# Kernel tuning notes

Hardware: AMD Instinct MI355X
Metric: run time of the kernel (lower is better)

## Reference

```python
import jax, jax.numpy as jnp
import numpy as np
from jax import lax

P = 8  # DFFN patch_size


def _ln(x, w, b):
    # WithBias LayerNorm over channel dim of NCHW (matches to_3d -> LN(-1) -> to_4d)
    mu = x.mean(1, keepdims=True)
    var = ((x - mu) ** 2).mean(1, keepdims=True)
    return (x - mu) / jnp.sqrt(var + 1e-5) * w[None, :, None, None] + b[None, :, None, None]


def _conv1x1(x, w, b=None):
    y = jnp.einsum('bchw,oc->bohw', x, w)
    if b is not None:
        y = y + b[None, :, None, None]
    return y


def setup_inputs() -> dict:
    key = jax.random.key(0)
    ks = jax.random.split(key, 9)
    B, C, H, W = 2, 64, 96, 96
    hid = C  # ffn_expansion_factor = 1
    s = lambda k, shape, scale=0.05: jax.random.normal(k, shape, jnp.float32) * scale
    return {
        'x': s(ks[0], (B, C, H, W), 1.0),
        'ln1_w': jnp.ones((C,), jnp.float32), 'ln1_b': jnp.zeros((C,), jnp.float32),
        'ln2_w': jnp.ones((C,), jnp.float32), 'ln2_b': jnp.zeros((C,), jnp.float32),
        'q_w': s(ks[1], (C, C)), 'q_b': jnp.zeros((C,), jnp.float32),
        'k_w': s(ks[2], (C, C)), 'k_b': jnp.zeros((C,), jnp.float32),
        'v_w': s(ks[3], (C, C)), 'v_b': jnp.zeros((C,), jnp.float32),
        'fft_w': s(ks[4], (hid, P, P // 2 + 1), 1.0),
        'proj_in_w': s(ks[5], (hid, C)),
        'dw_w': s(ks[6], (hid, 1, 3, 3)),
        'proj_out_w': s(ks[7], (C, hid // 2)),
    }


def reference(x, ln1_w, ln1_b, ln2_w, ln2_b, q_w, q_b, k_w, k_b, v_w, v_b,
              fft_w, proj_in_w, dw_w, proj_out_w):
    B, C, H, W = x.shape
    # --- attention sub-block (unscaled spatial self-attn) ---
    xn = _ln(x, ln1_w, ln1_b)
    q = _conv1x1(xn, q_w, q_b).reshape(B, C, H * W)
    k = _conv1x1(xn, k_w, k_b).reshape(B, C, H * W)
    v = _conv1x1(xn, v_w, v_b).reshape(B, C, H * W)
    attn = jax.nn.softmax(jnp.einsum('bcn,bcm->bnm', q, k), axis=-1)  # [B, HW, HW]
    out = jnp.einsum('bcm,bnm->bcn', v, attn).reshape(B, C, H, W)
    x = x + out
    # --- DFFN sub-block ---
    xn = _ln(x, ln2_w, ln2_b)
    h = _conv1x1(xn, proj_in_w)  # hidden == C (expansion factor 1)
    hid = h.shape[1]
    hb, wb = H // P, W // P
    hp = h.reshape(B, hid, hb, P, wb, P).transpose(0, 2, 4, 1, 3, 5)  # [B,hb,wb,hid,P,P]
    hf = jnp.fft.rfft2(hp) * fft_w  # real learned spectral filter
    hp = jnp.fft.irfft2(hf, s=(P, P))
    h = hp.transpose(0, 3, 1, 4, 2, 5).reshape(B, hid, H, W)
    h = lax.conv_general_dilated(h, dw_w, (1, 1), ((1, 1), (1, 1)),
                                 feature_group_count=hid,
                                 dimension_numbers=('NCHW', 'OIHW', 'NCHW'))
    h1, h2 = jnp.split(h, 2, axis=1)
    h = jax.nn.gelu(h1, approximate=False) * h2  # torch F.gelu is exact erf
    return x + _conv1x1(h, proj_out_w)
```

## Files before the change

kernel.cpp:

```cpp
#include <hip/hip_runtime.h>
#include <hip/hip_bf16.h>
#include <math.h>

#define CH 64
#define NPOS 9216
#define NTOT 18432
#define NSPLIT 12
#define TILES_PER_SPLIT 12
#define LOG2E 1.4426950408889634f

typedef short bf16x8 __attribute__((ext_vector_type(8)));
typedef short bf16x4 __attribute__((ext_vector_type(4)));
typedef float f32x4 __attribute__((ext_vector_type(4)));
typedef int   i32x4 __attribute__((ext_vector_type(4)));
typedef int   i32x2 __attribute__((ext_vector_type(2)));
typedef unsigned int u32;

__device__ __forceinline__ float bf2f(short s) {
  unsigned int u = ((unsigned int)(unsigned short)s) << 16;
  return __builtin_bit_cast(float, u);
}
__device__ __forceinline__ short f2bf(float f) {
  unsigned int u = __builtin_bit_cast(unsigned int, f);
  unsigned int r = (u + 0x7fffu + ((u >> 16) & 1u)) >> 16;
  return (short)r;
}
__device__ __forceinline__ float gelu_exact(float x) {
  return 0.5f * x * (1.f + erff(x * 0.70710678118654752440f));
}


__global__ __launch_bounds__(256) void k_ln_qkv(
    const float* __restrict__ x, const float* __restrict__ ln1w, const float* __restrict__ ln1b,
    const float* __restrict__ qw, const float* __restrict__ qb,
    const float* __restrict__ kw, const float* __restrict__ kb,
    const float* __restrict__ vw, const float* __restrict__ vb,
    short* __restrict__ Qg, short* __restrict__ Kg, short* __restrict__ Vgt) {
  __shared__ float s1a[256], s2a[256];
  __shared__ __align__(16) short xn[32 * 72];
  int t = threadIdx.x;
  int w8 = t >> 5;
  int p = t & 31;
  int q0 = blockIdx.x * 32;
  int q = q0 + p;
  int b = q / NPOS;
  int nn = q0 % NPOS;
  int n = q % NPOS;

  const float* xb = x + (size_t)b * CH * NPOS + n;
  float xr[8];
  float s1 = 0.f, s2 = 0.f;
#pragma unroll
  for (int cl = 0; cl < 8; ++cl) {
    float v = xb[(size_t)(w8 * 8 + cl) * NPOS];
    xr[cl] = v;
    s1 += v;
    s2 += v * v;
  }
  s1a[w8 * 32 + p] = s1;
  s2a[w8 * 32 + p] = s2;
  __syncthreads();
  float mu = 0.f, m2 = 0.f;
#pragma unroll
  for (int ww = 0; ww < 8; ++ww) { mu += s1a[ww * 32 + p]; m2 += s2a[ww * 32 + p]; }
  mu *= (1.f / 64.f);
  float var = m2 * (1.f / 64.f) - mu * mu;
  float rstd = rsqrtf(var + 1e-5f);
  {
    u32* xw = (u32*)xn;
#pragma unroll
    for (int j2 = 0; j2 < 4; ++j2) {
      int cl = 2 * j2, c = w8 * 8 + cl;
      float y0 = (xr[cl] - mu) * rstd * ln1w[c] + ln1b[c];
      float y1 = (xr[cl + 1] - mu) * rstd * ln1w[c + 1] + ln1b[c + 1];
      u32 pk = ((u32)(unsigned short)f2bf(y1) << 16) | (u32)(unsigned short)f2bf(y0);
      xw[p * 36 + w8 * 4 + j2] = pk;
    }
  }
  __syncthreads();
  int lane = t & 63;
  int L = lane & 15, quad = lane >> 4;
  int cs = t >> 6;
  bf16x8 b0[2], b1[2];
#pragma unroll
  for (int ps = 0; ps < 2; ++ps) {
    b0[ps] = *(const bf16x8*)(xn + (ps * 16 + L) * 72 + quad * 8);
    b1[ps] = *(const bf16x8*)(xn + (ps * 16 + L) * 72 + 32 + quad * 8);
  }
#pragma unroll
  for (int m = 0; m < 3; ++m) {
    const float* wsrc = (m == 0) ? qw : (m == 1) ? kw : vw;
    const float* bsrc = (m == 0) ? qb : (m == 1) ? kb : vb;
    bf16x8 a0, a1;
    {
      const float* wr = wsrc + (cs * 16 + L) * 64 + quad * 8;
#pragma unroll
      for (int j = 0; j < 8; ++j) { a0[j] = f2bf(wr[j]); a1[j] = f2bf(wr[32 + j]); }
    }
    float bi[4];
#pragma unroll
    for (int i = 0; i < 4; ++i) bi[i] = bsrc[cs * 16 + quad * 4 + i];
#pragma unroll
    for (int ps = 0; ps < 2; ++ps) {
      f32x4 acc = {bi[0], bi[1], bi[2], bi[3]};
      acc = __builtin_amdgcn_mfma_f32_16x16x32_bf16(a0, b0[ps], acc, 0, 0, 0);
      acc = __builtin_amdgcn_mfma_f32_16x16x32_bf16(a1, b1[ps], acc, 0, 0, 0);
      int idx = b * NPOS + nn + ps * 16 + L;
      if (m == 0) {
#pragma unroll
        for (int i = 0; i < 4; ++i)
          Qg[(size_t)idx * 64 + cs * 16 + quad * 4 + i] = f2bf(acc[i]);
      } else if (m == 1) {
#pragma unroll
        for (int i = 0; i < 4; ++i)
          Kg[(size_t)idx * 64 + cs * 16 + quad * 4 + i] = f2bf(acc[i] * LOG2E);
      } else {
#pragma unroll
        for (int i = 0; i < 4; ++i)
          Vgt[(size_t)(cs * 16 + quad * 4 + i) * NTOT + idx] = f2bf(acc[i]);
      }
    }
  }
}

#define LDPK 80
#define LDP  72
__global__ __launch_bounds__(512) void k_attn(
    const short* __restrict__ Qg, const short* __restrict__ Kg, const short* __restrict__ Vgt,
    u32* __restrict__ PoT, float* __restrict__ Pl) {
  __shared__ __align__(16) short Kt[2][64 * LDPK];
  __shared__ __align__(16) short Vt[2][64 * LDP];
  int b = blockIdx.y;
  int n0 = blockIdx.x * 256;
  int ks = blockIdx.z;
  int tid = threadIdx.x;
  int w = tid >> 6, lane = tid & 63;
  int L = lane & 15, quad = lane >> 4;

  bf16x8 qa[2][2];
#pragma unroll
  for (int qt = 0; qt < 2; ++qt) {
    const short* qb_ = Qg + ((size_t)(b * NPOS + n0 + w * 32 + qt * 16 + L)) * 64;
    qa[qt][0] = *(const bf16x8*)(qb_ + quad * 8);
    qa[qt][1] = *(const bf16x8*)(qb_ + 32 + quad * 8);
  }

  f32x4 o[2][4];
#pragma unroll
  for (int qt = 0; qt < 2; ++qt)
#pragma unroll
    for (int nb = 0; nb < 4; ++nb) o[qt][nb] = (f32x4){0.f, 0.f, 0.f, 0.f};
  float rl[2] = {0.f, 0.f};

  int ck = tid & 7, rk = tid >> 3;
  int c8 = tid & 7, dr = tid >> 3;
  int vslot = (c8 >> 2) * 32 + (c8 & 1) * 16 + ((c8 >> 1) & 1) * 4;
  i32x4 kr, vr;
  {
    int kt = ks * TILES_PER_SPLIT;
    kr = ((const i32x4*)(Kg + ((size_t)(b * NPOS + kt * 64)) * 64))[tid];
    vr = *(const i32x4*)(Vgt + (size_t)b * NPOS + kt * 64 + c8 * 8 + (size_t)dr * NTOT);
    ((i32x4*)Kt[0])[rk * 10 + ck] = kr;
    short* vrow = Vt[0] + dr * LDP + vslot;
    *(i32x2*)(vrow) = (i32x2){vr[0], vr[1]};
    *(i32x2*)(vrow + 8) = (i32x2){vr[2], vr[3]};
  }

  for (int t = 0; t < TILES_PER_SPLIT; ++t) {
    int cur = t & 1;
    if (t + 1 < TILES_PER_SPLIT) {
      int kt = ks * TILES_PER_SPLIT + t + 1;
      kr = ((const i32x4*)(Kg + ((size_t)(b * NPOS + kt * 64)) * 64))[tid];
      vr = *(const i32x4*)(Vgt + (size_t)b * NPOS + kt * 64 + c8 * 8 + (size_t)dr * NTOT);
    }
    __syncthreads();

    const i32x4* kt4 = (const i32x4*)Kt[cur];
    const short* vt = Vt[cur];
    __builtin_amdgcn_s_setprio(1);
#pragma unroll
    for (int kp = 0; kp < 2; ++kp) {
      u32 pw0[4], pw1[4];
#pragma unroll
      for (int h = 0; h < 2; ++h) {
        int kti = kp * 2 + h;
        bf16x8 kf0 = __builtin_bit_cast(bf16x8, kt4[(kti * 16 + L) * 10 + quad]);
        bf16x8 kf1 = __builtin_bit_cast(bf16x8, kt4[(kti * 16 + L) * 10 + 4 + quad]);
#pragma unroll
        for (int qt = 0; qt < 2; ++qt) {
          f32x4 st = {0.f, 0.f, 0.f, 0.f};
          st = __builtin_amdgcn_mfma_f32_16x16x32_bf16(kf0, qa[qt][0], st, 0, 0, 0);
          st = __builtin_amdgcn_mfma_f32_16x16x32_bf16(kf1, qa[qt][1], st, 0, 0, 0);
          float p0 = __builtin_amdgcn_exp2f(st[0]);
          float p1 = __builtin_amdgcn_exp2f(st[1]);
          float p2 = __builtin_amdgcn_exp2f(st[2]);
          float p3 = __builtin_amdgcn_exp2f(st[3]);
          rl[qt] += (p0 + p1) + (p2 + p3);
          u32 lo = __builtin_amdgcn_perm(__builtin_bit_cast(u32, p1), __builtin_bit_cast(u32, p0), 0x07060302u);
          u32 hi = __builtin_amdgcn_perm(__builtin_bit_cast(u32, p3), __builtin_bit_cast(u32, p2), 0x07060302u);
          if (qt == 0) { pw0[h * 2] = lo; pw0[h * 2 + 1] = hi; }
          else         { pw1[h * 2] = lo; pw1[h * 2 + 1] = hi; }
        }
      }
      i32x4 pq0 = {(int)pw0[0], (int)pw0[1], (int)pw0[2], (int)pw0[3]};
      i32x4 pq1 = {(int)pw1[0], (int)pw1[1], (int)pw1[2], (int)pw1[3]};
      bf16x8 pp0 = __builtin_bit_cast(bf16x8, pq0);
      bf16x8 pp1 = __builtin_bit_cast(bf16x8, pq1);
#pragma unroll
      for (int nb = 0; nb < 4; ++nb) {
        bf16x8 va8 = *(const bf16x8*)(vt + (nb * 16 + L) * LDP + kp * 32 + quad * 8);
        o[0][nb] = __builtin_amdgcn_mfma_f32_16x16x32_bf16(va8, pp0, o[0][nb], 0, 0, 0);
        o[1][nb] = __builtin_amdgcn_mfma_f32_16x16x32_bf16(va8, pp1, o[1][nb], 0, 0, 0);
      }
    }
    __builtin_amdgcn_s_setprio(0);

    if (t + 1 < TILES_PER_SPLIT) {
      int nxt = 1 - cur;
      ((i32x4*)Kt[nxt])[rk * 10 + ck] = kr;
      short* vrow = Vt[nxt] + dr * LDP + vslot;
      *(i32x2*)(vrow) = (i32x2){vr[0], vr[1]};
      *(i32x2*)(vrow + 8) = (i32x2){vr[2], vr[3]};
    }
  }

#pragma unroll
  for (int qt = 0; qt < 2; ++qt) {
    rl[qt] += __shfl_xor(rl[qt], 16);
    rl[qt] += __shfl_xor(rl[qt], 32);
  }

#pragma unroll
  for (int qt = 0; qt < 2; ++qt) {
    int qg = b * NPOS + n0 + w * 32 + qt * 16 + L;
#pragma unroll
    for (int nb = 0; nb < 4; ++nb)
#pragma unroll
      for (int ip = 0; ip < 2; ++ip) {
        u32 pk = ((u32)(unsigned short)f2bf(o[qt][nb][2 * ip + 1]) << 16) |
                 (u32)(unsigned short)f2bf(o[qt][nb][2 * ip]);
        int d32 = nb * 8 + quad * 2 + ip;
        PoT[((size_t)(ks * 32 + d32)) * NTOT + qg] = pk;
      }
    if (quad == 0) Pl[(size_t)ks * NTOT + qg] = rl[qt];
  }
}

__global__ __launch_bounds__(256) void k_res_ln2_proj(
    const float* __restrict__ x, const u32* __restrict__ PoT, const float* __restrict__ Pl,
    const float* __restrict__ ln2w, const float* __restrict__ ln2b,
    const float* __restrict__ piw,
    float* __restrict__ X2, float* __restrict__ Hbuf) {
  __shared__ float s1a[32 * 32], s2a[32 * 32];
  __shared__ float inva[32], mua[32], rsa[32];
  __shared__ __align__(16) short xn[32 * 72];
  int t = threadIdx.x;
  int q0 = blockIdx.x * 32;
  int b = q0 / NPOS;
  int nn = q0 % NPOS;

  if (t < 32) {
    float ls = 0.f;
#pragma unroll
    for (int s = 0; s < NSPLIT; ++s) ls += Pl[(size_t)s * NTOT + q0 + t];
    inva[t] = 1.f / ls;
  }
  __syncthreads();

  int rho = t >> 3;
  int p4 = (t & 7) * 4;
  int c0 = rho * 2;

  float aL[4] = {0.f, 0.f, 0.f, 0.f}, aH[4] = {0.f, 0.f, 0.f, 0.f};
#pragma unroll
  for (int s = 0; s < NSPLIT; ++s) {
    i32x4 v = *(const i32x4*)(PoT + (size_t)(s * 32 + rho) * NTOT + q0 + p4);
#pragma unroll
    for (int i = 0; i < 4; ++i) {
      u32 u = (u32)v[i];
      aL[i] += __builtin_bit_cast(float, u << 16);
      aH[i] += __builtin_bit_cast(float, u & 0xffff0000u);
    }
  }
  f32x4 x0 = *(const f32x4*)(x + (size_t)b * CH * NPOS + (size_t)c0 * NPOS + nn + p4);
  f32x4 x1 = *(const f32x4*)(x + (size_t)b * CH * NPOS + (size_t)(c0 + 1) * NPOS + nn + p4);
  float v0[4], v1[4];
  f32x4 ps1, ps2;
#pragma unroll
  for (int i = 0; i < 4; ++i) {
    float iv = inva[p4 + i];
    v0[i] = x0[i] + aL[i] * iv;
    v1[i] = x1[i] + aH[i] * iv;
    ps1[i] = v0[i] + v1[i];
    ps2[i] = v0[i] * v0[i] + v1[i] * v1[i];
  }
  *(f32x4*)&s1a[rho * 32 + p4] = ps1;
  *(f32x4*)&s2a[rho * 32 + p4] = ps2;
  {
    float* xo = X2 + (size_t)b * CH * NPOS + nn + p4;
    *(f32x4*)(xo + (size_t)c0 * NPOS) = (f32x4){v0[0], v0[1], v0[2], v0[3]};
    *(f32x4*)(xo + (size_t)(c0 + 1) * NPOS) = (f32x4){v1[0], v1[1], v1[2], v1[3]};
  }
  __syncthreads();
  if (t < 32) {
    float m = 0.f, m2 = 0.f;
#pragma unroll
    for (int r = 0; r < 32; ++r) { m += s1a[r * 32 + t]; m2 += s2a[r * 32 + t]; }
    m *= (1.f / 64.f);
    float var = m2 * (1.f / 64.f) - m * m;
    mua[t] = m;
    rsa[t] = rsqrtf(var + 1e-5f);
  }
  __syncthreads();
  {
    u32* xw = (u32*)xn;
    float w0 = ln2w[c0], w1 = ln2w[c0 + 1];
    float bb0 = ln2b[c0], bb1 = ln2b[c0 + 1];
#pragma unroll
    for (int i = 0; i < 4; ++i) {
      int p = p4 + i;
      float mu = mua[p], rs = rsa[p];
      float y0 = (v0[i] - mu) * rs * w0 + bb0;
      float y1 = (v1[i] - mu) * rs * w1 + bb1;
      xw[p * 36 + rho] = ((u32)(unsigned short)f2bf(y1) << 16) | (u32)(unsigned short)f2bf(y0);
    }
  }
  __syncthreads();
  int lane = t & 63;
  int L = lane & 15, quad = lane >> 4;
  int cs = t >> 6;
  bf16x8 a0, a1;
  {
    const float* wr = piw + (cs * 16 + L) * 64 + quad * 8;
#pragma unroll
    for (int j = 0; j < 8; ++j) { a0[j] = f2bf(wr[j]); a1[j] = f2bf(wr[32 + j]); }
  }
  float* hb = Hbuf + (size_t)b * CH * NPOS + nn;
#pragma unroll
  for (int ps = 0; ps < 2; ++ps) {
    bf16x8 b0 = *(const bf16x8*)(xn + (ps * 16 + L) * 72 + quad * 8);
    bf16x8 b1 = *(const bf16x8*)(xn + (ps * 16 + L) * 72 + 32 + quad * 8);
    f32x4 acc = {0.f, 0.f, 0.f, 0.f};
    acc = __builtin_amdgcn_mfma_f32_16x16x32_bf16(a0, b0, acc, 0, 0, 0);
    acc = __builtin_amdgcn_mfma_f32_16x16x32_bf16(a1, b1, acc, 0, 0, 0);
#pragma unroll
    for (int i = 0; i < 4; ++i)
      hb[(size_t)(cs * 16 + quad * 4 + i) * NPOS + ps * 16 + L] = acc[i];
  }
}

#define LDB 100
__global__ __launch_bounds__(96) void k_conv(
    float* __restrict__ Hbuf, const float* __restrict__ fftw) {
  __shared__ __align__(16) float band[8 * LDB];
  __shared__ float kl[64];
  int hb = blockIdx.x, c = blockIdx.y, b = blockIdx.z;
  int t = threadIdx.x;
  float* base = Hbuf + (size_t)(b * CH + c) * NPOS + hb * 8 * 96;
  if (t < 64) {
    int dp = t >> 3, dq = t & 7;
    const float r = 0.70710678118654752440f;
    const float CO[8] = {1.f, r, 0.f, -r, -1.f, -r, 0.f, r};
    const float* wc = fftw + c * 40;
    float acc = 0.f;
#pragma unroll
    for (int u = 0; u < 8; ++u) {
#pragma unroll
      for (int v = 0; v < 8; ++v) {
        float wv = (v <= 4) ? wc[u * 5 + v] : wc[((8 - u) & 7) * 5 + (8 - v)];
        acc += wv * CO[(u * dp + v * dq) & 7];
      }
    }
    kl[t] = acc * (1.f / 64.f);
  }
  {
    int sr = t / 12, sc = (t % 12) * 8;
    f32x4 a = *(const f32x4*)(base + sr * 96 + sc);
    f32x4 d = *(const f32x4*)(base + sr * 96 + sc + 4);
    *(f32x4*)&band[sr * LDB + sc] = a;
    *(f32x4*)&band[sr * LDB + sc + 4] = d;
  }
  __syncthreads();
  int p = t / 12, wb = t % 12;
  float out[8] = {0.f, 0.f, 0.f, 0.f, 0.f, 0.f, 0.f, 0.f};
#pragma unroll
  for (int dp = 0; dp < 8; ++dp) {
    int rr = (p - dp) & 7;
    f32x4 a = *(const f32x4*)&band[rr * LDB + wb * 8];
    f32x4 d = *(const f32x4*)&band[rr * LDB + wb * 8 + 4];
    float v[8] = {a[0], a[1], a[2], a[3], d[0], d[1], d[2], d[3]};
    const float* krow = &kl[dp * 8];
#pragma unroll
    for (int dq = 0; dq < 8; ++dq) {
      float kv = krow[dq];
#pragma unroll
      for (int q = 0; q < 8; ++q) out[q] += kv * v[(q - dq) & 7];
    }
  }
  __syncthreads();
  f32x4 w0 = {out[0], out[1], out[2], out[3]};
  f32x4 w1 = {out[4], out[5], out[6], out[7]};
  *(f32x4*)(base + p * 96 + wb * 8) = w0;
  *(f32x4*)(base + p * 96 + wb * 8 + 4) = w1;
}

__global__ __launch_bounds__(256) void k_dw_gate(
    const float* __restrict__ Hbuf, const float* __restrict__ dww,
    float* __restrict__ G) {
  int cc = blockIdx.y;
  int q = blockIdx.x * 256 + threadIdx.x;
  int b = q / NPOS, n = q % NPOS;
  int y = n / 96, xx = n % 96;
  const float* h1 = Hbuf + (size_t)(b * CH + cc) * NPOS;
  const float* h2 = Hbuf + (size_t)(b * CH + cc + 32) * NPOS;
  float wd1[9], wd2[9];
#pragma unroll
  for (int ki = 0; ki < 9; ++ki) { wd1[ki] = dww[cc * 9 + ki]; wd2[ki] = dww[(cc + 32) * 9 + ki]; }
  float d1 = 0.f, d2 = 0.f;
  for (int dy = -1; dy <= 1; ++dy) {
    int yy = y + dy;
    if (yy < 0 || yy >= 96) continue;
    for (int dx = -1; dx <= 1; ++dx) {
      int xv = xx + dx;
      if (xv < 0 || xv >= 96) continue;
      int ki = (dy + 1) * 3 + (dx + 1);
      d1 += h1[yy * 96 + xv] * wd1[ki];
      d2 += h2[yy * 96 + xv] * wd2[ki];
    }
  }
  G[(size_t)cc * NTOT + q] = gelu_exact(d1) * d2;
}

__global__ __launch_bounds__(256) void k_proj_out(
    const float* __restrict__ G, const float* __restrict__ poww,
    const float* __restrict__ X2, float* __restrict__ out) {
  int og = blockIdx.y;
  int q = blockIdx.x * 256 + threadIdx.x;
  int b = q / NPOS, n = q % NPOS;
  float g[32];
#pragma unroll
  for (int cg = 0; cg < 32; ++cg) g[cg] = G[(size_t)cg * NTOT + q];
  const float* xr = X2 + (size_t)b * CH * NPOS + n;
  float* ob = out + (size_t)b * CH * NPOS + n;
#pragma unroll
  for (int j = 0; j < 4; ++j) {
    int oc = og * 4 + j;
    const float* prow = poww + oc * 32;
    float acc = xr[(size_t)oc * NPOS];
#pragma unroll
    for (int cg = 0; cg < 32; ++cg) acc += prow[cg] * g[cg];
    ob[(size_t)oc * NPOS] = acc;
  }
}

extern "C" void kernel_launch(void* const* d_in, const int* in_sizes, int n_in,
                              void* d_out, int out_size, void* d_ws, size_t ws_size,
                              hipStream_t stream) {
  const float* x    = (const float*)d_in[0];
  const float* ln1w = (const float*)d_in[1];
  const float* ln1b = (const float*)d_in[2];
  const float* ln2w = (const float*)d_in[3];
  const float* ln2b = (const float*)d_in[4];
  const float* qw   = (const float*)d_in[5];
  const float* qb   = (const float*)d_in[6];
  const float* kw   = (const float*)d_in[7];
  const float* kb   = (const float*)d_in[8];
  const float* vw   = (const float*)d_in[9];
  const float* vb   = (const float*)d_in[10];
  const float* fftw = (const float*)d_in[11];
  const float* piw  = (const float*)d_in[12];
  const float* dww  = (const float*)d_in[13];
  const float* poww = (const float*)d_in[14];

  short* Qg  = (short*)d_ws;
  short* Kg  = Qg + (size_t)NTOT * 64;
  short* Vgt = Kg + (size_t)NTOT * 64;
  u32*   PoT = (u32*)(Vgt + (size_t)NTOT * 64);
  float* Pl  = (float*)(PoT + (size_t)NSPLIT * 32 * NTOT);
  float* X2  = Pl + (size_t)NSPLIT * NTOT;
  float* Hbuf = X2 + (size_t)NTOT * 64;
  float* G   = Hbuf + (size_t)NTOT * 64;

  k_ln_qkv<<<dim3(576), 256, 0, stream>>>(x, ln1w, ln1b, qw, qb, kw, kb, vw, vb, Qg, Kg, Vgt);
  k_attn<<<dim3(36, 2, NSPLIT), 512, 0, stream>>>(Qg, Kg, Vgt, PoT, Pl);
  k_res_ln2_proj<<<dim3(576), 256, 0, stream>>>(x, PoT, Pl, ln2w, ln2b, piw, X2, Hbuf);
  k_conv<<<dim3(12, 64, 2), 96, 0, stream>>>(Hbuf, fftw);
  k_dw_gate<<<dim3(72, 32), 256, 0, stream>>>(Hbuf, dww, G);
  k_proj_out<<<dim3(72, 16), 256, 0, stream>>>(G, poww, X2, (float*)d_out);
}
```

Measured before the change: 169.6 us.

## Split attention tile compute around LDS prefetch store; vectorize depthwise gate

In the attention kernel, the per-tile compute is split into two halves, and the store of the prefetched next K/V tile into shared memory is placed between them. This overlaps the LDS writes with MFMA work instead of leaving them after all compute. Separately, the depthwise 3x3 conv plus gate kernel now handles four adjacent pixels per thread using vector loads and shifted neighbor vectors, with a quarter of the blocks. This cuts per-pixel load and index overhead, at the cost of more registers per thread and fewer threads in flight.

```diff
diff --git a/kernel.cpp b/kernel.cpp
--- a/kernel.cpp
+++ b/kernel.cpp
@@ -177,9 +177,7 @@
 
     const i32x4* kt4 = (const i32x4*)Kt[cur];
     const short* vt = Vt[cur];
-    __builtin_amdgcn_s_setprio(1);
-#pragma unroll
-    for (int kp = 0; kp < 2; ++kp) {
+    auto compute_win = [&](int kp) {
       u32 pw0[4], pw1[4];
 #pragma unroll
       for (int h = 0; h < 2; ++h) {
@@ -212,7 +210,10 @@
         o[0][nb] = __builtin_amdgcn_mfma_f32_16x16x32_bf16(va8, pp0, o[0][nb], 0, 0, 0);
         o[1][nb] = __builtin_amdgcn_mfma_f32_16x16x32_bf16(va8, pp1, o[1][nb], 0, 0, 0);
       }
-    }
+    };
+
+    __builtin_amdgcn_s_setprio(1);
+    compute_win(0);
     __builtin_amdgcn_s_setprio(0);
 
     if (t + 1 < TILES_PER_SPLIT) {
@@ -222,6 +223,10 @@
       *(i32x2*)(vrow) = (i32x2){vr[0], vr[1]};
       *(i32x2*)(vrow + 8) = (i32x2){vr[2], vr[3]};
     }
+
+    __builtin_amdgcn_s_setprio(1);
+    compute_win(1);
+    __builtin_amdgcn_s_setprio(0);
   }
 
 #pragma unroll
@@ -408,27 +413,39 @@
     const float* __restrict__ Hbuf, const float* __restrict__ dww,
     float* __restrict__ G) {
   int cc = blockIdx.y;
-  int q = blockIdx.x * 256 + threadIdx.x;
-  int b = q / NPOS, n = q % NPOS;
-  int y = n / 96, xx = n % 96;
+  int q4 = (blockIdx.x * 256 + threadIdx.x) * 4;
+  int b = q4 / NPOS, n = q4 % NPOS;
+  int y = n / 96, x0 = n % 96;
   const float* h1 = Hbuf + (size_t)(b * CH + cc) * NPOS;
   const float* h2 = Hbuf + (size_t)(b * CH + cc + 32) * NPOS;
   float wd1[9], wd2[9];
 #pragma unroll
   for (int ki = 0; ki < 9; ++ki) { wd1[ki] = dww[cc * 9 + ki]; wd2[ki] = dww[(cc + 32) * 9 + ki]; }
-  float d1 = 0.f, d2 = 0.f;
+  f32x4 d1 = {0.f, 0.f, 0.f, 0.f}, d2 = {0.f, 0.f, 0.f, 0.f};
+#pragma unroll
   for (int dy = -1; dy <= 1; ++dy) {
     int yy = y + dy;
     if (yy < 0 || yy >= 96) continue;
-    for (int dx = -1; dx <= 1; ++dx) {
-      int xv = xx + dx;
-      if (xv < 0 || xv >= 96) continue;
-      int ki = (dy + 1) * 3 + (dx + 1);
-      d1 += h1[yy * 96 + xv] * wd1[ki];
-      d2 += h2[yy * 96 + xv] * wd2[ki];
-    }
-  }
-  G[(size_t)cc * NTOT + q] = gelu_exact(d1) * d2;
+    const float* r1 = h1 + yy * 96 + x0;
+    const float* r2 = h2 + yy * 96 + x0;
+    f32x4 c1 = *(const f32x4*)r1;
+    f32x4 c2 = *(const f32x4*)r2;
+    float l1 = (x0 > 0) ? r1[-1] : 0.f;
+    float l2 = (x0 > 0) ? r2[-1] : 0.f;
+    float rr1 = (x0 + 4 < 96) ? r1[4] : 0.f;
+    float rr2 = (x0 + 4 < 96) ? r2[4] : 0.f;
+    int kb = (dy + 1) * 3;
+    f32x4 L1 = {l1, c1[0], c1[1], c1[2]};
+    f32x4 R1 = {c1[1], c1[2], c1[3], rr1};
+    f32x4 L2 = {l2, c2[0], c2[1], c2[2]};
+    f32x4 R2 = {c2[1], c2[2], c2[3], rr2};
+    d1 += L1 * wd1[kb] + c1 * wd1[kb + 1] + R1 * wd1[kb + 2];
+    d2 += L2 * wd2[kb] + c2 * wd2[kb + 1] + R2 * wd2[kb + 2];
+  }
+  f32x4 gv;
+#pragma unroll
+  for (int i = 0; i < 4; ++i) gv[i] = gelu_exact(d1[i]) * d2[i];
+  *(f32x4*)(G + (size_t)cc * NTOT + q4) = gv;
 }
 
 __global__ __launch_bounds__(256) void k_proj_out(
@@ -485,6 +502,6 @@
   k_attn<<<dim3(36, 2, NSPLIT), 512, 0, stream>>>(Qg, Kg, Vgt, PoT, Pl);
   k_res_ln2_proj<<<dim3(576), 256, 0, stream>>>(x, PoT, Pl, ln2w, ln2b, piw, X2, Hbuf);
   k_conv<<<dim3(12, 64, 2), 96, 0, stream>>>(Hbuf, fftw);
-  k_dw_gate<<<dim3(72, 32), 256, 0, stream>>>(Hbuf, dww, G);
+  k_dw_gate<<<dim3(18, 32), 256, 0, stream>>>(Hbuf, dww, G);
   k_proj_out<<<dim3(72, 16), 256, 0, stream>>>(G, poww, X2, (float*)d_out);
 }
```

Measured after the change: 164.9 us. 1.03x faster.
